# Optimization experiments

Measured on AMD Instinct MI355X. Metric: run time of the kernel, lower is better.

Reference implementation:

```python
import jax, jax.numpy as jnp
import numpy as np

B = 32          # batch
IH = IW = 32    # image_size
N = IH * IW     # tokens = 1024
INP = 256
OUP = 256
H = 8           # heads
D = 32          # dim_head
INNER = H * D   # 256
TABLE = (2 * IH - 1) * (2 * IW - 1)  # 3969


def _rel_index():
    # exact replica of the torch buffer construction
    coords = np.stack(np.meshgrid(np.arange(IH), np.arange(IW), indexing='ij')).reshape(2, -1)
    rel = coords[:, :, None] - coords[:, None, :]
    rel[0] += IH - 1
    rel[1] += IW - 1
    rel[0] *= 2 * IW - 1
    return (rel[0] + rel[1]).reshape(-1)  # [N*N]


def setup_inputs() -> dict:
    key = jax.random.key(0)
    k0, k1, k2, k3 = jax.random.split(key, 4)
    x = jax.random.normal(k0, (B, N, INP), jnp.float32)
    W_qkv = jax.random.normal(k1, (INP, 3 * INNER), jnp.float32) * 0.02
    bias_table = jax.random.normal(k2, (TABLE, H), jnp.float32) * 0.02
    W_out = jax.random.normal(k3, (INNER, OUP), jnp.float32) * 0.02
    b_out = jnp.zeros((OUP,), jnp.float32)
    rel_index = jnp.asarray(_rel_index(), jnp.int32)
    return {"x": x, "W_qkv": W_qkv, "bias_table": bias_table,
            "W_out": W_out, "b_out": b_out, "rel_index": rel_index}


def reference(x, W_qkv, bias_table, W_out, b_out, rel_index):
    scale = D ** -0.5
    qkv = x @ W_qkv                                   # [B, N, 3*INNER]
    q, k, v = jnp.split(qkv, 3, axis=-1)
    to_heads = lambda t: t.reshape(B, N, H, D).transpose(0, 2, 1, 3)  # b h n d
    q, k, v = to_heads(q), to_heads(k), to_heads(v)
    dots = jnp.einsum('bhid,bhjd->bhij', q, k) * scale  # [B, H, N, N]
    # gather per-head relative position bias: [N*N, H] -> [1, H, N, N]
    bias = bias_table[rel_index].reshape(N, N, H).transpose(2, 0, 1)[None]
    attn = jax.nn.softmax(dots + bias, axis=-1)
    out = jnp.einsum('bhij,bhjd->bhid', attn, v)        # [B, H, N, D]
    out = out.transpose(0, 2, 1, 3).reshape(B, N, INNER)
    return out @ W_out + b_out
```

## Files before the change

### kernel.cpp

```cpp
#include <hip/hip_runtime.h>

typedef __attribute__((ext_vector_type(4))) int            vi4;
typedef __attribute__((ext_vector_type(4))) float          vf4;
typedef __attribute__((ext_vector_type(8))) short          vs8;
typedef __attribute__((ext_vector_type(2))) unsigned int   vu2;
typedef unsigned short u16;
typedef unsigned int   u32;

#define LOG2E  1.4426950408889634f
#define QSCALE 0.2550484109f

static __device__ __forceinline__ u16 f2bf(float f) {
  u32 u = __builtin_bit_cast(u32, f);
  u32 r = (u + 0x7fffu + ((u >> 16) & 1u)) >> 16;
  return (u16)r;
}
static __device__ __forceinline__ float bfu_lo(u32 u) {
  return __builtin_bit_cast(float, u << 16);
}
static __device__ __forceinline__ float bfu_hi(u32 u) {
  return __builtin_bit_cast(float, u & 0xffff0000u);
}
static __device__ __forceinline__ u32 packbf_perm(float a, float b) {
  return __builtin_amdgcn_perm(__builtin_bit_cast(u32, b),
                               __builtin_bit_cast(u32, a), 0x07060302u);
}

static __device__ __forceinline__ void ldsdma16(void* lds, const void* g) {
  __builtin_amdgcn_global_load_lds(
      (const u32 __attribute__((address_space(1)))*)g,
      (u32 __attribute__((address_space(3)))*)lds, 16, 0, 0);
}

__global__ void prep_all(const float* __restrict__ x, u16* __restrict__ xbf,
                         const float* __restrict__ Wqkv, u16* __restrict__ WqkvT,
                         const float* __restrict__ Wout, u16* __restrict__ WoutT,
                         const int* __restrict__ rel, const float* __restrict__ table,
                         u32* __restrict__ bias_pk, float* __restrict__ bias_f,
                         int use_f32) {
  __shared__ __align__(8) u16 relS[64 * 32];
  int bid = blockIdx.x, tid = threadIdx.x;
  if (bid < 8192) {
    int i = (bid * 256 + tid) * 4;
    vf4 v = *(const vf4*)&x[i];
    u32 lo = (u32)f2bf(v[0]) | ((u32)f2bf(v[1]) << 16);
    u32 hi = (u32)f2bf(v[2]) | ((u32)f2bf(v[3]) << 16);
    vu2 o; o[0] = lo; o[1] = hi;
    *(vu2*)&xbf[i] = o;
  } else if (bid < 9216) {
    const float* src; u16* dst; int C, idx;
    if (bid < 8960) { src = Wqkv; dst = WqkvT; C = 768; idx = (bid - 8192) * 256 + tid; }
    else            { src = Wout; dst = WoutT; C = 256; idx = (bid - 8960) * 256 + tid; }
    int r = idx / C, c = idx - r * C;
    dst[c * 256 + r] = f2bf(src[idx]);
  } else {
    int b2 = bid - 9216;
    int qt = b2 >> 6, t = (b2 >> 2) & 15, s = b2 & 3;
    int ti = s >> 1, jhalf = s & 1;
    int wave = tid >> 6, quad = (tid >> 4) & 3, l15 = tid & 15;
    int jbase = t * 64 + jhalf * 32;

#pragma unroll
    for (int p = 0; p < 2; ++p) {
      int task = p * 256 + tid;
      int q = task >> 3, unit = task & 7;
      int m = qt * 128 + (q >> 4) * 32 + ti * 16 + (q & 15);
      vi4 v = *(const vi4*)&rel[m * 1024 + jbase + unit * 4];
      vu2 pk;
      pk[0] = (u32)(v[0] & 0xffff) | ((u32)v[1] << 16);
      pk[1] = (u32)(v[2] & 0xffff) | ((u32)v[3] << 16);
      *(vu2*)&relS[q * 32 + unit * 4] = pk;
    }
    __syncthreads();

    int mrow = wave * 16 + l15;
    float vals[8][8];
#pragma unroll
    for (int tjl = 0; tjl < 2; ++tjl)
#pragma unroll
      for (int r = 0; r < 4; ++r) {
        int idx = relS[mrow * 32 + tjl * 16 + quad * 4 + r];
        vf4 a = *(const vf4*)&table[idx * 8];
        vf4 bb = *(const vf4*)&table[idx * 8 + 4];
#pragma unroll
        for (int h = 0; h < 4; ++h) {
          vals[tjl * 4 + r][h] = a[h];
          vals[tjl * 4 + r][h + 4] = bb[h];
        }
      }
    if (use_f32) {
#pragma unroll
      for (int h = 0; h < 8; ++h)
#pragma unroll
        for (int tjl = 0; tjl < 2; ++tjl) {
          int frag = ti * 4 + jhalf * 2 + tjl;
          vf4 v;
#pragma unroll
          for (int r = 0; r < 4; ++r) v[r] = vals[tjl * 4 + r][h] * LOG2E;
          *(vf4*)&bias_f[(((h * 8 + qt) * 16 + t) * 8 + frag) * 1024 + tid * 4] = v;
        }
    } else {
#pragma unroll
      for (int h = 0; h < 8; ++h) {
        u32 o[4];
#pragma unroll
        for (int tjl = 0; tjl < 2; ++tjl)
#pragma unroll
          for (int p = 0; p < 2; ++p) {
            u32 lo = f2bf(vals[tjl * 4 + 2 * p][h] * LOG2E);
            u32 hi = f2bf(vals[tjl * 4 + 2 * p + 1][h] * LOG2E);
            o[tjl * 2 + p] = lo | (hi << 16);
          }
        *(vi4*)&bias_pk[h * 524288 + (qt * 16 + t) * 4096 + tid * 16 + s * 4] =
            *(const vi4*)o;
      }
    }
  }
}

template <int EPI>
__global__ __launch_bounds__(256, 2) void gemm_k256(
    const u16* __restrict__ A, const u16* __restrict__ Bt,
    u16* __restrict__ q_out, u16* __restrict__ k_out, u16* __restrict__ v_out,
    float* __restrict__ c_out, const float* __restrict__ bias) {
  __shared__ __align__(16) u16 SMEM[EPI == 0 ? 128 * 136 : 8192];
  u16* As = SMEM;
  u16* Bs = SMEM + 4096;
  const int tid = threadIdx.x;
  const int lane15 = tid & 15, quad = (tid >> 4) & 3, wave = tid >> 6;
  const int wr = (wave & 1) * 64, wc = (wave >> 1) * 64;
  const int m0 = blockIdx.y * 128, n0 = blockIdx.x * 128;

  const u16* Ag = &A[(m0 + (tid >> 2)) * 256 + (tid & 3) * 8];
  const u16* Bg = &Bt[(n0 + (tid >> 2)) * 256 + (tid & 3) * 8];
  u16* AsW = &As[wave * 512];
  u16* BsW = &Bs[wave * 512];

  const vf4 z4 = {0.f, 0.f, 0.f, 0.f};
  vf4 acc[4][4];
#pragma unroll
  for (int i = 0; i < 4; ++i)
#pragma unroll
    for (int j = 0; j < 4; ++j) acc[i][j] = z4;

  for (int k0 = 0; k0 < 256; k0 += 32) {
    __syncthreads();
    ldsdma16(AsW,        Ag + k0);
    ldsdma16(AsW + 2048, Ag + k0 + 64 * 256);
    ldsdma16(BsW,        Bg + k0);
    ldsdma16(BsW + 2048, Bg + k0 + 64 * 256);
    __syncthreads();
    vs8 af[4], bfr[4];
#pragma unroll
    for (int ti = 0; ti < 4; ++ti)
      af[ti] = *(const vs8*)&As[(wr + ti * 16 + lane15) * 32 + quad * 8];
#pragma unroll
    for (int tj = 0; tj < 4; ++tj)
      bfr[tj] = *(const vs8*)&Bs[(wc + tj * 16 + lane15) * 32 + quad * 8];
#pragma unroll
    for (int ti = 0; ti < 4; ++ti)
#pragma unroll
      for (int tj = 0; tj < 4; ++tj)
        acc[ti][tj] = __builtin_amdgcn_mfma_f32_16x16x32_bf16(af[ti], bfr[tj],
                                                              acc[ti][tj], 0, 0, 0);
  }

  if (EPI == 0) {
    const int which = n0 >> 8;
    const int bb = m0 >> 10, nn0 = m0 & 1023;
    u16* Cs = SMEM;
    __syncthreads();
    if (which < 2) {
      float sc = (which == 0) ? QSCALE : 1.f;
#pragma unroll
      for (int tj = 0; tj < 4; ++tj) {
        int col = wc + tj * 16 + lane15;
#pragma unroll
        for (int ti = 0; ti < 4; ++ti) {
          int row0 = wr + ti * 16 + quad * 4;
#pragma unroll
          for (int r = 0; r < 4; ++r)
            Cs[(row0 + r) * 136 + col] = f2bf(acc[ti][tj][r] * sc);
        }
      }
      __syncthreads();
      u16* base = (which == 0) ? q_out : k_out;
#pragma unroll
      for (int hp = 0; hp < 4; ++hp) {
        int hh = ((n0 + hp * 32) >> 5) & 7;
        u16* pb = base + ((bb * 8 + hh) * 1024 + nn0) * 32;
#pragma unroll
        for (int p2 = 0; p2 < 2; ++p2) {
          int task = p2 * 256 + tid;
          int row = task >> 2, unit = task & 3;
          vi4 v = *(const vi4*)&Cs[row * 136 + hp * 32 + unit * 8];
          *(vi4*)&pb[row * 32 + unit * 8] = v;
        }
      }
    } else {
#pragma unroll
      for (int tj = 0; tj < 4; ++tj) {
        int col = wc + tj * 16 + lane15;
#pragma unroll
        for (int ti = 0; ti < 4; ++ti) {
          int row0 = wr + ti * 16 + quad * 4;
          vu2 pk;
          pk[0] = (u32)f2bf(acc[ti][tj][0]) | ((u32)f2bf(acc[ti][tj][1]) << 16);
          pk[1] = (u32)f2bf(acc[ti][tj][2]) | ((u32)f2bf(acc[ti][tj][3]) << 16);
          *(vu2*)&Cs[col * 136 + row0] = pk;
        }
      }
      __syncthreads();
#pragma unroll
      for (int p = 0; p < 8; ++p) {
        int task = p * 256 + tid;
        int col = task >> 4, unit = task & 15;
        int cg = n0 + col;
        int hh = (cg >> 5) & 7, d = cg & 31;
        vi4 v = *(const vi4*)&Cs[col * 136 + unit * 8];
        *(vi4*)&v_out[((bb * 8 + hh) * 32 + d) * 1024 + nn0 + unit * 8] = v;
      }
    }
  } else {
#pragma unroll
    for (int tj = 0; tj < 4; ++tj) {
      int colg = n0 + wc + tj * 16 + lane15;
      float bo = bias[colg];
#pragma unroll
      for (int ti = 0; ti < 4; ++ti)
#pragma unroll
        for (int r = 0; r < 4; ++r) {
          int rowg = m0 + wr + ti * 16 + quad * 4 + r;
          c_out[rowg * 256 + colg] = acc[ti][tj][r] + bo;
        }
    }
  }
}

template <int BF32>
__global__ __launch_bounds__(256, 4) void flash_attn(
    const u16* __restrict__ Qws, const u16* __restrict__ Kws,
    const u16* __restrict__ Vtws, const void* __restrict__ biasv,
    u16* __restrict__ Ows) {
  __shared__ __align__(16) u16 Qs[128 * 32];
  __shared__ __align__(16) u16 Ks[64 * 40];
  __shared__ __align__(16) u16 Vt[32 * 72];
  __shared__ __align__(16) u16 Ps[4][32 * 72];

  const int tid = threadIdx.x;
  const int l15 = tid & 15, quad = (tid >> 4) & 3, wave = tid >> 6;
  const int bid = blockIdx.x;
  const int h = bid & 7, b = (bid >> 3) & 31, qt = bid >> 8;
  const int q0 = qt * 128;
  const int bh = b * 8 + h;
  const u16* Qbase = Qws + (bh * 1024 + q0) * 32;
  const u16* Kbase = Kws + bh * 1024 * 32;
  const u16* Vbase = Vtws + bh * 32 * 1024;
  const u32* Bpk = (const u32*)biasv + h * 524288 + qt * 65536 + tid * 16;
  const float* Bf = (const float*)biasv + (h * 8 + qt) * 131072 + tid * 4;

  const int kv_j = tid >> 2, kv_seg = (tid & 3) * 8;
  const int v_d = tid >> 3,  v_seg = (tid & 7) * 8;
  const u16* Kg = Kbase + kv_j * 32 + kv_seg;
  const u16* Vg = Vbase + v_d * 1024 + v_seg;

  ldsdma16(&Qs[wave * 512],        Qbase + tid * 8);
  ldsdma16(&Qs[2048 + wave * 512], Qbase + 2048 + tid * 8);

  vi4 kreg = *(const vi4*)Kg;
  vi4 vreg = *(const vi4*)Vg;

  __syncthreads();
  vs8 af[2];
#pragma unroll
  for (int ti = 0; ti < 2; ++ti)
    af[ti] = *(const vs8*)&Qs[(wave * 32 + ti * 16 + l15) * 32 + quad * 8];

  const vf4 z4 = {0.f, 0.f, 0.f, 0.f};
  vf4 O[2][2];
  O[0][0] = z4; O[0][1] = z4; O[1][0] = z4; O[1][1] = z4;
  vf4 Lacc[2];
  Lacc[0] = z4; Lacc[1] = z4;

  vs8 onesv;
#pragma unroll
  for (int i = 0; i < 8; ++i) onesv[i] = (short)0x3F80;

  u16* PwBase = Ps[wave];

  for (int t = 0; t < 16; ++t) {
    __syncthreads();
    *(vi4*)&Ks[kv_j * 40 + kv_seg] = kreg;
    *(vi4*)&Vt[v_d * 72 + v_seg] = vreg;
    __syncthreads();

    if (t < 15) {
      kreg = *(const vi4*)(Kg + (t + 1) * 2048);
      vreg = *(const vi4*)(Vg + (t + 1) * 64);
    }

    vi4 bld[4];
    if (!BF32) {
#pragma unroll
      for (int i = 0; i < 4; ++i) bld[i] = *(const vi4*)(Bpk + t * 4096 + i * 4);
    }
    const u32* bl = (const u32*)bld;

    vs8 bk[4];
#pragma unroll
    for (int tj = 0; tj < 4; ++tj)
      bk[tj] = *(const vs8*)&Ks[(tj * 16 + l15) * 40 + quad * 8];

#pragma unroll
    for (int ti = 0; ti < 2; ++ti)
#pragma unroll
      for (int tj = 0; tj < 4; ++tj) {
        vf4 c;
        if (BF32) {
          c = *(const vf4*)&Bf[(t * 8 + ti * 4 + tj) * 1024];
        } else {
          u32 b0 = bl[(ti * 4 + tj) * 2], b1 = bl[(ti * 4 + tj) * 2 + 1];
          c[0] = bfu_lo(b0); c[1] = bfu_hi(b0);
          c[2] = bfu_lo(b1); c[3] = bfu_hi(b1);
        }
        vf4 st = __builtin_amdgcn_mfma_f32_16x16x32_bf16(bk[tj], af[ti], c, 0, 0, 0);
        float p0 = __builtin_exp2f(st[0]);
        float p1 = __builtin_exp2f(st[1]);
        float p2 = __builtin_exp2f(st[2]);
        float p3 = __builtin_exp2f(st[3]);
        vu2 pk; pk[0] = packbf_perm(p0, p1); pk[1] = packbf_perm(p2, p3);
        *(vu2*)&PwBase[(ti * 16 + l15) * 72 + tj * 16 + quad * 4] = pk;
      }

#pragma unroll
    for (int kk = 0; kk < 2; ++kk) {
      vs8 pf[2], bv[2];
#pragma unroll
      for (int ti = 0; ti < 2; ++ti)
        pf[ti] = *(const vs8*)&PwBase[(ti * 16 + l15) * 72 + kk * 32 + quad * 8];
#pragma unroll
      for (int tj2 = 0; tj2 < 2; ++tj2)
        bv[tj2] = *(const vs8*)&Vt[(tj2 * 16 + l15) * 72 + kk * 32 + quad * 8];
#pragma unroll
      for (int ti = 0; ti < 2; ++ti) {
#pragma unroll
        for (int tj2 = 0; tj2 < 2; ++tj2)
          O[ti][tj2] = __builtin_amdgcn_mfma_f32_16x16x32_bf16(bv[tj2], pf[ti],
                                                               O[ti][tj2], 0, 0, 0);
        Lacc[ti] = __builtin_amdgcn_mfma_f32_16x16x32_bf16(onesv, pf[ti],
                                                           Lacc[ti], 0, 0, 0);
      }
    }
  }

#pragma unroll
  for (int ti = 0; ti < 2; ++ti) {
    float inv = __builtin_amdgcn_rcpf(Lacc[ti][0]);
    int m = q0 + wave * 32 + ti * 16 + l15;
    int rowbase = (b * 1024 + m) * 256 + h * 32;
#pragma unroll
    for (int tj2 = 0; tj2 < 2; ++tj2) {
      u32 lo = (u32)f2bf(O[ti][tj2][0] * inv) | ((u32)f2bf(O[ti][tj2][1] * inv) << 16);
      u32 hi = (u32)f2bf(O[ti][tj2][2] * inv) | ((u32)f2bf(O[ti][tj2][3] * inv) << 16);
      vu2 pk; pk[0] = lo; pk[1] = hi;
      *(vu2*)&Ows[rowbase + tj2 * 16 + quad * 4] = pk;
    }
  }
}

extern "C" void kernel_launch(void* const* d_in, const int* in_sizes, int n_in,
                              void* d_out, int out_size, void* d_ws, size_t ws_size,
                              hipStream_t stream) {
  (void)in_sizes; (void)n_in; (void)out_size;
  const float* x     = (const float*)d_in[0];
  const float* Wqkv  = (const float*)d_in[1];
  const float* table = (const float*)d_in[2];
  const float* Wout  = (const float*)d_in[3];
  const float* bout  = (const float*)d_in[4];
  const int*   rel   = (const int*)d_in[5];
  float* out = (float*)d_out;

  const int use_f32 = (ws_size >= 101187584ull) ? 1 : 0;
  const size_t bias_bytes = use_f32 ? 33554432ull : 16777216ull;

  char* ws = (char*)d_ws;
  u16* xbf    = (u16*)(ws);
  u16* Qws    = (u16*)(ws + 16777216);
  u16* Kws    = (u16*)(ws + 33554432);
  u16* Vtws   = (u16*)(ws + 50331648);
  void* biasp = (void*)(ws + 67108864);
  u16* WqkvT  = (u16*)(ws + 67108864 + bias_bytes);
  u16* WoutT  = WqkvT + 196608;

  prep_all<<<9728, 256, 0, stream>>>(x, xbf, Wqkv, WqkvT, Wout, WoutT,
                                     rel, table, (u32*)biasp, (float*)biasp,
                                     use_f32);
  gemm_k256<0><<<dim3(6, 256), 256, 0, stream>>>(xbf, WqkvT, Qws, Kws, Vtws,
                                                 nullptr, nullptr);
  if (use_f32)
    flash_attn<1><<<2048, 256, 0, stream>>>(Qws, Kws, Vtws, biasp, xbf);
  else
    flash_attn<0><<<2048, 256, 0, stream>>>(Qws, Kws, Vtws, biasp, xbf);
  gemm_k256<1><<<dim3(2, 256), 256, 0, stream>>>(xbf, WoutT,
                                                 nullptr, nullptr, nullptr, out, bout);
}
```

Baseline: 229.6 us.

## Double-buffer K/V tiles in LDS and prefetch bias one step ahead

Makes the K and V shared-memory tiles double-buffered, so the next tile is written after the PV MFMAs and each iteration needs only one barrier instead of two. Half of the bias values are now prefetched one iteration ahead and split into two phases, so the bias loads overlap with the QK and PV work. Q fragments are loaded straight from global memory into registers, which removes the Q LDS staging and its barrier. The cost is more LDS for K/V and more live registers for the prefetched bias, which may lower occupancy under launch_bounds(256,4).

```diff
diff --git a/kernel.cpp b/kernel.cpp
--- a/kernel.cpp
+++ b/kernel.cpp
@@ -24,6 +24,12 @@
 static __device__ __forceinline__ u32 packbf_perm(float a, float b) {
   return __builtin_amdgcn_perm(__builtin_bit_cast(u32, b),
                                __builtin_bit_cast(u32, a), 0x07060302u);
+}
+static __device__ __forceinline__ vf4 unpack_bias(const u32* grp, int tj) {
+  u32 b0 = grp[tj * 2], b1 = grp[tj * 2 + 1];
+  vf4 c; c[0] = bfu_lo(b0); c[1] = bfu_hi(b0);
+  c[2] = bfu_lo(b1); c[3] = bfu_hi(b1);
+  return c;
 }
 
 static __device__ __forceinline__ void ldsdma16(void* lds, const void* g) {
@@ -242,9 +248,8 @@
     const u16* __restrict__ Qws, const u16* __restrict__ Kws,
     const u16* __restrict__ Vtws, const void* __restrict__ biasv,
     u16* __restrict__ Ows) {
-  __shared__ __align__(16) u16 Qs[128 * 32];
-  __shared__ __align__(16) u16 Ks[64 * 40];
-  __shared__ __align__(16) u16 Vt[32 * 72];
+  __shared__ __align__(16) u16 Ks[2][64 * 40];
+  __shared__ __align__(16) u16 Vt[2][32 * 72];
   __shared__ __align__(16) u16 Ps[4][32 * 72];
 
   const int tid = threadIdx.x;
@@ -256,25 +261,33 @@
   const u16* Qbase = Qws + (bh * 1024 + q0) * 32;
   const u16* Kbase = Kws + bh * 1024 * 32;
   const u16* Vbase = Vtws + bh * 32 * 1024;
-  const u32* Bpk = (const u32*)biasv + h * 524288 + qt * 65536 + tid * 16;
   const float* Bf = (const float*)biasv + (h * 8 + qt) * 131072 + tid * 4;
+  const u32*  Bpk = (const u32*)biasv + h * 524288 + qt * 65536 + tid * 16;
 
   const int kv_j = tid >> 2, kv_seg = (tid & 3) * 8;
   const int v_d = tid >> 3,  v_seg = (tid & 7) * 8;
   const u16* Kg = Kbase + kv_j * 32 + kv_seg;
   const u16* Vg = Vbase + v_d * 1024 + v_seg;
 
-  ldsdma16(&Qs[wave * 512],        Qbase + tid * 8);
-  ldsdma16(&Qs[2048 + wave * 512], Qbase + 2048 + tid * 8);
+  vs8 af[2];
+#pragma unroll
+  for (int ti = 0; ti < 2; ++ti)
+    af[ti] = *(const vs8*)&Qbase[(wave * 32 + ti * 16 + l15) * 32 + quad * 8];
 
   vi4 kreg = *(const vi4*)Kg;
   vi4 vreg = *(const vi4*)Vg;
-
-  __syncthreads();
-  vs8 af[2];
-#pragma unroll
-  for (int ti = 0; ti < 2; ++ti)
-    af[ti] = *(const vs8*)&Qs[(wave * 32 + ti * 16 + l15) * 32 + quad * 8];
+  *(vi4*)&Ks[0][kv_j * 40 + kv_seg] = kreg;
+  *(vi4*)&Vt[0][v_d * 72 + v_seg] = vreg;
+
+  vf4 b0pre[4];
+  vi4 bpk_pre[2];
+  if (BF32) {
+#pragma unroll
+    for (int i = 0; i < 4; ++i) b0pre[i] = *(const vf4*)&Bf[i * 1024];
+  } else {
+#pragma unroll
+    for (int i = 0; i < 2; ++i) bpk_pre[i] = *(const vi4*)(Bpk + i * 4);
+  }
 
   const vf4 z4 = {0.f, 0.f, 0.f, 0.f};
   vf4 O[2][2];
@@ -289,48 +302,60 @@
   u16* PwBase = Ps[wave];
 
   for (int t = 0; t < 16; ++t) {
-    __syncthreads();
-    *(vi4*)&Ks[kv_j * 40 + kv_seg] = kreg;
-    *(vi4*)&Vt[v_d * 72 + v_seg] = vreg;
+    const int cur = t & 1, nxt = cur ^ 1;
     __syncthreads();
 
     if (t < 15) {
       kreg = *(const vi4*)(Kg + (t + 1) * 2048);
       vreg = *(const vi4*)(Vg + (t + 1) * 64);
     }
-
-    vi4 bld[4];
-    if (!BF32) {
-#pragma unroll
-      for (int i = 0; i < 4; ++i) bld[i] = *(const vi4*)(Bpk + t * 4096 + i * 4);
-    }
-    const u32* bl = (const u32*)bld;
+    vf4 b1cur[4], b0nxt[4];
+    vi4 bpk1[2], bpk_n[2];
+    if (BF32) {
+#pragma unroll
+      for (int i = 0; i < 4; ++i)
+        b1cur[i] = *(const vf4*)&Bf[(t * 8 + 4 + i) * 1024];
+      if (t < 15) {
+#pragma unroll
+        for (int i = 0; i < 4; ++i)
+          b0nxt[i] = *(const vf4*)&Bf[((t + 1) * 8 + i) * 1024];
+      }
+    } else {
+      bpk1[0] = *(const vi4*)(Bpk + t * 4096 + 8);
+      bpk1[1] = *(const vi4*)(Bpk + t * 4096 + 12);
+      if (t < 15) {
+        bpk_n[0] = *(const vi4*)(Bpk + (t + 1) * 4096);
+        bpk_n[1] = *(const vi4*)(Bpk + (t + 1) * 4096 + 4);
+      }
+    }
 
     vs8 bk[4];
 #pragma unroll
     for (int tj = 0; tj < 4; ++tj)
-      bk[tj] = *(const vs8*)&Ks[(tj * 16 + l15) * 40 + quad * 8];
-
-#pragma unroll
-    for (int ti = 0; ti < 2; ++ti)
-#pragma unroll
-      for (int tj = 0; tj < 4; ++tj) {
-        vf4 c;
-        if (BF32) {
-          c = *(const vf4*)&Bf[(t * 8 + ti * 4 + tj) * 1024];
-        } else {
-          u32 b0 = bl[(ti * 4 + tj) * 2], b1 = bl[(ti * 4 + tj) * 2 + 1];
-          c[0] = bfu_lo(b0); c[1] = bfu_hi(b0);
-          c[2] = bfu_lo(b1); c[3] = bfu_hi(b1);
-        }
-        vf4 st = __builtin_amdgcn_mfma_f32_16x16x32_bf16(bk[tj], af[ti], c, 0, 0, 0);
-        float p0 = __builtin_exp2f(st[0]);
-        float p1 = __builtin_exp2f(st[1]);
-        float p2 = __builtin_exp2f(st[2]);
-        float p3 = __builtin_exp2f(st[3]);
-        vu2 pk; pk[0] = packbf_perm(p0, p1); pk[1] = packbf_perm(p2, p3);
-        *(vu2*)&PwBase[(ti * 16 + l15) * 72 + tj * 16 + quad * 4] = pk;
-      }
+      bk[tj] = *(const vs8*)&Ks[cur][(tj * 16 + l15) * 40 + quad * 8];
+
+#pragma unroll
+    for (int tj = 0; tj < 4; ++tj) {
+      vf4 c = BF32 ? b0pre[tj] : unpack_bias((const u32*)bpk_pre, tj);
+      vf4 st = __builtin_amdgcn_mfma_f32_16x16x32_bf16(bk[tj], af[0], c, 0, 0, 0);
+      float p0 = __builtin_exp2f(st[0]);
+      float p1 = __builtin_exp2f(st[1]);
+      float p2 = __builtin_exp2f(st[2]);
+      float p3 = __builtin_exp2f(st[3]);
+      vu2 pk; pk[0] = packbf_perm(p0, p1); pk[1] = packbf_perm(p2, p3);
+      *(vu2*)&PwBase[l15 * 72 + tj * 16 + quad * 4] = pk;
+    }
+#pragma unroll
+    for (int tj = 0; tj < 4; ++tj) {
+      vf4 c = BF32 ? b1cur[tj] : unpack_bias((const u32*)bpk1, tj);
+      vf4 st = __builtin_amdgcn_mfma_f32_16x16x32_bf16(bk[tj], af[1], c, 0, 0, 0);
+      float p0 = __builtin_exp2f(st[0]);
+      float p1 = __builtin_exp2f(st[1]);
+      float p2 = __builtin_exp2f(st[2]);
+      float p3 = __builtin_exp2f(st[3]);
+      vu2 pk; pk[0] = packbf_perm(p0, p1); pk[1] = packbf_perm(p2, p3);
+      *(vu2*)&PwBase[(16 + l15) * 72 + tj * 16 + quad * 4] = pk;
+    }
 
 #pragma unroll
     for (int kk = 0; kk < 2; ++kk) {
@@ -340,7 +365,7 @@
         pf[ti] = *(const vs8*)&PwBase[(ti * 16 + l15) * 72 + kk * 32 + quad * 8];
 #pragma unroll
       for (int tj2 = 0; tj2 < 2; ++tj2)
-        bv[tj2] = *(const vs8*)&Vt[(tj2 * 16 + l15) * 72 + kk * 32 + quad * 8];
+        bv[tj2] = *(const vs8*)&Vt[cur][(tj2 * 16 + l15) * 72 + kk * 32 + quad * 8];
 #pragma unroll
       for (int ti = 0; ti < 2; ++ti) {
 #pragma unroll
@@ -349,6 +374,17 @@
                                                                O[ti][tj2], 0, 0, 0);
         Lacc[ti] = __builtin_amdgcn_mfma_f32_16x16x32_bf16(onesv, pf[ti],
                                                            Lacc[ti], 0, 0, 0);
+      }
+    }
+
+    if (t < 15) {
+      *(vi4*)&Ks[nxt][kv_j * 40 + kv_seg] = kreg;
+      *(vi4*)&Vt[nxt][v_d * 72 + v_seg] = vreg;
+      if (BF32) {
+#pragma unroll
+        for (int i = 0; i < 4; ++i) b0pre[i] = b0nxt[i];
+      } else {
+        bpk_pre[0] = bpk_n[0]; bpk_pre[1] = bpk_n[1];
       }
     }
   }
```

Result: no change. 225.6 us (-1.7%).

## Double-buffer K/V in LDS and prefetch bias in flash attention

Applied to the files above, without the earlier changes.

Rewrites the attention loop to double-buffer K/V tiles in shared memory, which leaves one barrier per tile instead of two. It prefetches the next tile's bias registers and loads Q straight into registers instead of going through LDS. It also drops the fp32 bias path, so bias is always stored as packed bf16 and the workspace layout is fixed. This adds register pressure and lowers bias precision when the workspace is large.

```diff
diff --git a/kernel.cpp b/kernel.cpp
--- a/kernel.cpp
+++ b/kernel.cpp
@@ -36,8 +36,7 @@
                          const float* __restrict__ Wqkv, u16* __restrict__ WqkvT,
                          const float* __restrict__ Wout, u16* __restrict__ WoutT,
                          const int* __restrict__ rel, const float* __restrict__ table,
-                         u32* __restrict__ bias_pk, float* __restrict__ bias_f,
-                         int use_f32) {
+                         u32* __restrict__ bias_pk) {
   __shared__ __align__(8) u16 relS[64 * 32];
   int bid = blockIdx.x, tid = threadIdx.x;
   if (bid < 8192) {
@@ -88,32 +87,19 @@
           vals[tjl * 4 + r][h + 4] = bb[h];
         }
       }
-    if (use_f32) {
-#pragma unroll
-      for (int h = 0; h < 8; ++h)
-#pragma unroll
-        for (int tjl = 0; tjl < 2; ++tjl) {
-          int frag = ti * 4 + jhalf * 2 + tjl;
-          vf4 v;
-#pragma unroll
-          for (int r = 0; r < 4; ++r) v[r] = vals[tjl * 4 + r][h] * LOG2E;
-          *(vf4*)&bias_f[(((h * 8 + qt) * 16 + t) * 8 + frag) * 1024 + tid * 4] = v;
-        }
-    } else {
-#pragma unroll
-      for (int h = 0; h < 8; ++h) {
-        u32 o[4];
-#pragma unroll
-        for (int tjl = 0; tjl < 2; ++tjl)
-#pragma unroll
-          for (int p = 0; p < 2; ++p) {
-            u32 lo = f2bf(vals[tjl * 4 + 2 * p][h] * LOG2E);
-            u32 hi = f2bf(vals[tjl * 4 + 2 * p + 1][h] * LOG2E);
-            o[tjl * 2 + p] = lo | (hi << 16);
-          }
-        *(vi4*)&bias_pk[h * 524288 + (qt * 16 + t) * 4096 + tid * 16 + s * 4] =
-            *(const vi4*)o;
-      }
+#pragma unroll
+    for (int h = 0; h < 8; ++h) {
+      u32 o[4];
+#pragma unroll
+      for (int tjl = 0; tjl < 2; ++tjl)
+#pragma unroll
+        for (int p = 0; p < 2; ++p) {
+          u32 lo = f2bf(vals[tjl * 4 + 2 * p][h] * LOG2E);
+          u32 hi = f2bf(vals[tjl * 4 + 2 * p + 1][h] * LOG2E);
+          o[tjl * 2 + p] = lo | (hi << 16);
+        }
+      *(vi4*)&bias_pk[h * 524288 + (qt * 16 + t) * 4096 + tid * 16 + s * 4] =
+          *(const vi4*)o;
     }
   }
 }
@@ -237,15 +223,68 @@
   }
 }
 
-template <int BF32>
+#define MFMA_BF16 __builtin_amdgcn_mfma_f32_16x16x32_bf16
+
+#define QK_TILE(AF, PTOFF, U0, U1)                                         \
+  {                                                                        \
+    vf4 c; c[0] = bfu_lo(U0); c[1] = bfu_hi(U0);                           \
+    c[2] = bfu_lo(U1); c[3] = bfu_hi(U1);                                  \
+    vf4 st = MFMA_BF16(bk[_tj], AF, c, 0, 0, 0);                           \
+    float p0 = __builtin_exp2f(st[0]);                                     \
+    float p1 = __builtin_exp2f(st[1]);                                     \
+    float p2 = __builtin_exp2f(st[2]);                                     \
+    float p3 = __builtin_exp2f(st[3]);                                     \
+    vu2 pk; pk[0] = packbf_perm(p0, p1); pk[1] = packbf_perm(p2, p3);      \
+    *(vu2*)&L[pwb + (PTOFF) + _tj * 16] = pk;                              \
+  }
+
+#define FLASH_HALF(T, CUR, NXT, BC0, BC1, BN0, BN1, LAST)                  \
+  {                                                                        \
+    vi4 b1a = *(const vi4*)(Bpk + (T) * 4096 + 8);                         \
+    vi4 b1b = *(const vi4*)(Bpk + (T) * 4096 + 12);                        \
+    if (!(LAST)) {                                                         \
+      kreg = *(const vi4*)(Kg + ((T) + 1) * 2048);                         \
+      vreg = *(const vi4*)(Vg + ((T) + 1) * 64);                           \
+      BN0 = *(const vi4*)(Bpk + ((T) + 1) * 4096);                         \
+      BN1 = *(const vi4*)(Bpk + ((T) + 1) * 4096 + 4);                     \
+    }                                                                      \
+    __syncthreads();                                                       \
+    vs8 bk[4];                                                             \
+    _Pragma("unroll") for (int _tj = 0; _tj < 4; ++_tj)                    \
+        bk[_tj] = *(const vs8*)&L[bkb + (CUR) * 2560 + _tj * 640];         \
+    _Pragma("unroll") for (int _tj = 0; _tj < 4; ++_tj) {                  \
+      u32 u0 = (_tj < 2) ? (u32)BC0[_tj * 2] : (u32)BC1[(_tj - 2) * 2];    \
+      u32 u1 = (_tj < 2) ? (u32)BC0[_tj * 2 + 1] : (u32)BC1[(_tj - 2) * 2 + 1]; \
+      QK_TILE(af0, 0, u0, u1)                                              \
+    }                                                                      \
+    _Pragma("unroll") for (int _tj = 0; _tj < 4; ++_tj) {                  \
+      u32 u0 = (_tj < 2) ? (u32)b1a[_tj * 2] : (u32)b1b[(_tj - 2) * 2];    \
+      u32 u1 = (_tj < 2) ? (u32)b1a[_tj * 2 + 1] : (u32)b1b[(_tj - 2) * 2 + 1]; \
+      QK_TILE(af1, 1152, u0, u1)                                           \
+    }                                                                      \
+    _Pragma("unroll") for (int kk = 0; kk < 2; ++kk) {                     \
+      vs8 pf0 = *(const vs8*)&L[pfb + kk * 32];                            \
+      vs8 pf1 = *(const vs8*)&L[pfb + 1152 + kk * 32];                     \
+      vs8 bv0 = *(const vs8*)&L[bvb + (CUR) * 2304 + kk * 32];             \
+      vs8 bv1 = *(const vs8*)&L[bvb + (CUR) * 2304 + 1152 + kk * 32];      \
+      O00 = MFMA_BF16(bv0, pf0, O00, 0, 0, 0);                             \
+      O01 = MFMA_BF16(bv1, pf0, O01, 0, 0, 0);                             \
+      La0 = MFMA_BF16(onesv, pf0, La0, 0, 0, 0);                           \
+      O10 = MFMA_BF16(bv0, pf1, O10, 0, 0, 0);                             \
+      O11 = MFMA_BF16(bv1, pf1, O11, 0, 0, 0);                             \
+      La1 = MFMA_BF16(onesv, pf1, La1, 0, 0, 0);                           \
+    }                                                                      \
+    if (!(LAST)) {                                                         \
+      *(vi4*)&L[ksw + (NXT) * 2560] = kreg;                                \
+      *(vi4*)&L[vsw + (NXT) * 2304] = vreg;                                \
+    }                                                                      \
+  }
+
 __global__ __launch_bounds__(256, 4) void flash_attn(
     const u16* __restrict__ Qws, const u16* __restrict__ Kws,
-    const u16* __restrict__ Vtws, const void* __restrict__ biasv,
+    const u16* __restrict__ Vtws, const u32* __restrict__ bias_pk,
     u16* __restrict__ Ows) {
-  __shared__ __align__(16) u16 Qs[128 * 32];
-  __shared__ __align__(16) u16 Ks[64 * 40];
-  __shared__ __align__(16) u16 Vt[32 * 72];
-  __shared__ __align__(16) u16 Ps[4][32 * 72];
+  __shared__ __align__(16) u16 L[18944];
 
   const int tid = threadIdx.x;
   const int l15 = tid & 15, quad = (tid >> 4) & 3, wave = tid >> 6;
@@ -254,116 +293,63 @@
   const int q0 = qt * 128;
   const int bh = b * 8 + h;
   const u16* Qbase = Qws + (bh * 1024 + q0) * 32;
-  const u16* Kbase = Kws + bh * 1024 * 32;
-  const u16* Vbase = Vtws + bh * 32 * 1024;
-  const u32* Bpk = (const u32*)biasv + h * 524288 + qt * 65536 + tid * 16;
-  const float* Bf = (const float*)biasv + (h * 8 + qt) * 131072 + tid * 4;
-
-  const int kv_j = tid >> 2, kv_seg = (tid & 3) * 8;
-  const int v_d = tid >> 3,  v_seg = (tid & 7) * 8;
-  const u16* Kg = Kbase + kv_j * 32 + kv_seg;
-  const u16* Vg = Vbase + v_d * 1024 + v_seg;
-
-  ldsdma16(&Qs[wave * 512],        Qbase + tid * 8);
-  ldsdma16(&Qs[2048 + wave * 512], Qbase + 2048 + tid * 8);
+  const u16* Kg = Kws + bh * 1024 * 32 + (tid >> 2) * 32 + (tid & 3) * 8;
+  const u16* Vg = Vtws + bh * 32 * 1024 + (tid >> 3) * 1024 + (tid & 7) * 8;
+  const u32* Bpk = bias_pk + h * 524288 + qt * 65536 + tid * 16;
+
+  const int ksw = (tid >> 2) * 40 + (tid & 3) * 8;
+  const int vsw = 5120 + (tid >> 3) * 72 + (tid & 7) * 8;
+  const int bkb = l15 * 40 + quad * 8;
+  const int bvb = 5120 + l15 * 72 + quad * 8;
+  const int pfb = 9728 + wave * 2304 + l15 * 72 + quad * 8;
+  const int pwb = 9728 + wave * 2304 + l15 * 72 + quad * 4;
+
+  vs8 af0 = *(const vs8*)&Qbase[(wave * 32 + l15) * 32 + quad * 8];
+  vs8 af1 = *(const vs8*)&Qbase[(wave * 32 + 16 + l15) * 32 + quad * 8];
 
   vi4 kreg = *(const vi4*)Kg;
   vi4 vreg = *(const vi4*)Vg;
-
-  __syncthreads();
-  vs8 af[2];
-#pragma unroll
-  for (int ti = 0; ti < 2; ++ti)
-    af[ti] = *(const vs8*)&Qs[(wave * 32 + ti * 16 + l15) * 32 + quad * 8];
+  *(vi4*)&L[ksw] = kreg;
+  *(vi4*)&L[vsw] = vreg;
+  vi4 bA0 = *(const vi4*)(Bpk);
+  vi4 bA1 = *(const vi4*)(Bpk + 4);
+  vi4 bB0 = bA0, bB1 = bA1;
 
   const vf4 z4 = {0.f, 0.f, 0.f, 0.f};
-  vf4 O[2][2];
-  O[0][0] = z4; O[0][1] = z4; O[1][0] = z4; O[1][1] = z4;
-  vf4 Lacc[2];
-  Lacc[0] = z4; Lacc[1] = z4;
+  vf4 O00 = z4, O01 = z4, O10 = z4, O11 = z4;
+  vf4 La0 = z4, La1 = z4;
 
   vs8 onesv;
 #pragma unroll
   for (int i = 0; i < 8; ++i) onesv[i] = (short)0x3F80;
 
-  u16* PwBase = Ps[wave];
-
-  for (int t = 0; t < 16; ++t) {
-    __syncthreads();
-    *(vi4*)&Ks[kv_j * 40 + kv_seg] = kreg;
-    *(vi4*)&Vt[v_d * 72 + v_seg] = vreg;
-    __syncthreads();
-
-    if (t < 15) {
-      kreg = *(const vi4*)(Kg + (t + 1) * 2048);
-      vreg = *(const vi4*)(Vg + (t + 1) * 64);
-    }
-
-    vi4 bld[4];
-    if (!BF32) {
-#pragma unroll
-      for (int i = 0; i < 4; ++i) bld[i] = *(const vi4*)(Bpk + t * 4096 + i * 4);
-    }
-    const u32* bl = (const u32*)bld;
-
-    vs8 bk[4];
-#pragma unroll
-    for (int tj = 0; tj < 4; ++tj)
-      bk[tj] = *(const vs8*)&Ks[(tj * 16 + l15) * 40 + quad * 8];
-
-#pragma unroll
-    for (int ti = 0; ti < 2; ++ti)
-#pragma unroll
-      for (int tj = 0; tj < 4; ++tj) {
-        vf4 c;
-        if (BF32) {
-          c = *(const vf4*)&Bf[(t * 8 + ti * 4 + tj) * 1024];
-        } else {
-          u32 b0 = bl[(ti * 4 + tj) * 2], b1 = bl[(ti * 4 + tj) * 2 + 1];
-          c[0] = bfu_lo(b0); c[1] = bfu_hi(b0);
-          c[2] = bfu_lo(b1); c[3] = bfu_hi(b1);
-        }
-        vf4 st = __builtin_amdgcn_mfma_f32_16x16x32_bf16(bk[tj], af[ti], c, 0, 0, 0);
-        float p0 = __builtin_exp2f(st[0]);
-        float p1 = __builtin_exp2f(st[1]);
-        float p2 = __builtin_exp2f(st[2]);
-        float p3 = __builtin_exp2f(st[3]);
-        vu2 pk; pk[0] = packbf_perm(p0, p1); pk[1] = packbf_perm(p2, p3);
-        *(vu2*)&PwBase[(ti * 16 + l15) * 72 + tj * 16 + quad * 4] = pk;
-      }
-
-#pragma unroll
-    for (int kk = 0; kk < 2; ++kk) {
-      vs8 pf[2], bv[2];
-#pragma unroll
-      for (int ti = 0; ti < 2; ++ti)
-        pf[ti] = *(const vs8*)&PwBase[(ti * 16 + l15) * 72 + kk * 32 + quad * 8];
-#pragma unroll
-      for (int tj2 = 0; tj2 < 2; ++tj2)
-        bv[tj2] = *(const vs8*)&Vt[(tj2 * 16 + l15) * 72 + kk * 32 + quad * 8];
-#pragma unroll
-      for (int ti = 0; ti < 2; ++ti) {
-#pragma unroll
-        for (int tj2 = 0; tj2 < 2; ++tj2)
-          O[ti][tj2] = __builtin_amdgcn_mfma_f32_16x16x32_bf16(bv[tj2], pf[ti],
-                                                               O[ti][tj2], 0, 0, 0);
-        Lacc[ti] = __builtin_amdgcn_mfma_f32_16x16x32_bf16(onesv, pf[ti],
-                                                           Lacc[ti], 0, 0, 0);
-      }
-    }
-  }
-
-#pragma unroll
-  for (int ti = 0; ti < 2; ++ti) {
-    float inv = __builtin_amdgcn_rcpf(Lacc[ti][0]);
-    int m = q0 + wave * 32 + ti * 16 + l15;
-    int rowbase = (b * 1024 + m) * 256 + h * 32;
+  for (int tt = 0; tt < 8; ++tt) {
+    const int t0 = tt * 2, t1 = tt * 2 + 1;
+    FLASH_HALF(t0, 0, 1, bA0, bA1, bB0, bB1, 0)
+    FLASH_HALF(t1, 1, 0, bB0, bB1, bA0, bA1, (tt == 7))
+  }
+
+  {
+    float inv0 = __builtin_amdgcn_rcpf(La0[0]);
+    float inv1 = __builtin_amdgcn_rcpf(La1[0]);
+    int m0 = q0 + wave * 32 + l15;
+    int rb0 = (b * 1024 + m0) * 256 + h * 32;
+    int rb1 = (b * 1024 + m0 + 16) * 256 + h * 32;
 #pragma unroll
     for (int tj2 = 0; tj2 < 2; ++tj2) {
-      u32 lo = (u32)f2bf(O[ti][tj2][0] * inv) | ((u32)f2bf(O[ti][tj2][1] * inv) << 16);
-      u32 hi = (u32)f2bf(O[ti][tj2][2] * inv) | ((u32)f2bf(O[ti][tj2][3] * inv) << 16);
-      vu2 pk; pk[0] = lo; pk[1] = hi;
-      *(vu2*)&Ows[rowbase + tj2 * 16 + quad * 4] = pk;
+      vu2 pk;
+      pk[0] = packbf_perm(O00[0] * inv0, O00[1] * inv0);
+      pk[1] = packbf_perm(O00[2] * inv0, O00[3] * inv0);
+      vu2 qk;
+      const vf4& oo = (tj2 == 0) ? O00 : O01;
+      qk[0] = packbf_perm(oo[0] * inv0, oo[1] * inv0);
+      qk[1] = packbf_perm(oo[2] * inv0, oo[3] * inv0);
+      *(vu2*)&Ows[rb0 + tj2 * 16 + quad * 4] = qk;
+      const vf4& o1 = (tj2 == 0) ? O10 : O11;
+      vu2 rk;
+      rk[0] = packbf_perm(o1[0] * inv1, o1[1] * inv1);
+      rk[1] = packbf_perm(o1[2] * inv1, o1[3] * inv1);
+      *(vu2*)&Ows[rb1 + tj2 * 16 + quad * 4] = rk;
     }
   }
 }
@@ -371,7 +357,7 @@
 extern "C" void kernel_launch(void* const* d_in, const int* in_sizes, int n_in,
                               void* d_out, int out_size, void* d_ws, size_t ws_size,
                               hipStream_t stream) {
-  (void)in_sizes; (void)n_in; (void)out_size;
+  (void)in_sizes; (void)n_in; (void)out_size; (void)ws_size;
   const float* x     = (const float*)d_in[0];
   const float* Wqkv  = (const float*)d_in[1];
   const float* table = (const float*)d_in[2];
@@ -380,27 +366,20 @@
   const int*   rel   = (const int*)d_in[5];
   float* out = (float*)d_out;
 
-  const int use_f32 = (ws_size >= 101187584ull) ? 1 : 0;
-  const size_t bias_bytes = use_f32 ? 33554432ull : 16777216ull;
-
   char* ws = (char*)d_ws;
   u16* xbf    = (u16*)(ws);
   u16* Qws    = (u16*)(ws + 16777216);
   u16* Kws    = (u16*)(ws + 33554432);
   u16* Vtws   = (u16*)(ws + 50331648);
-  void* biasp = (void*)(ws + 67108864);
-  u16* WqkvT  = (u16*)(ws + 67108864 + bias_bytes);
-  u16* WoutT  = WqkvT + 196608;
+  u32* biaspk = (u32*)(ws + 67108864);
+  u16* WqkvT  = (u16*)(ws + 83886080);
+  u16* WoutT  = (u16*)(ws + 84279296);
 
   prep_all<<<9728, 256, 0, stream>>>(x, xbf, Wqkv, WqkvT, Wout, WoutT,
-                                     rel, table, (u32*)biasp, (float*)biasp,
-                                     use_f32);
+                                     rel, table, biaspk);
   gemm_k256<0><<<dim3(6, 256), 256, 0, stream>>>(xbf, WqkvT, Qws, Kws, Vtws,
                                                  nullptr, nullptr);
-  if (use_f32)
-    flash_attn<1><<<2048, 256, 0, stream>>>(Qws, Kws, Vtws, biasp, xbf);
-  else
-    flash_attn<0><<<2048, 256, 0, stream>>>(Qws, Kws, Vtws, biasp, xbf);
+  flash_attn<<<2048, 256, 0, stream>>>(Qws, Kws, Vtws, biaspk, xbf);
   gemm_k256<1><<<dim3(2, 256), 256, 0, stream>>>(xbf, WoutT,
                                                  nullptr, nullptr, nullptr, out, bout);
 }
```

After: 237.1 us. 1.03x slower.
